# Optimization experiments

Hardware: AMD Instinct MI355X
Metric: run time of the kernel (lower is better)

The kernel has to match this reference:

```python
import jax, jax.numpy as jnp
import numpy as np

B, N, D = 4, 1024, 1024
H, KV, HD = 16, 4, 64
S, CTX = 128, 2048
MLPD = 4096
NITER, DT = 2, 0.1


def _rms(x, w, eps=1e-6):
    return x * jax.lax.rsqrt(jnp.mean(x * x, axis=-1, keepdims=True) + eps) * w


def _gelu(x):
    return jax.nn.gelu(x, approximate=False)  # torch nn.GELU() is exact erf


def _rope(q, k, cos, sin):
    # q: [B,H,N,HD], cos/sin: [N, HD//2]; interleaved-half RoPE as in source
    q1, q2 = q[..., ::2], q[..., 1::2]
    k1, k2 = k[..., ::2], k[..., 1::2]
    c = cos[None, None]
    s = sin[None, None]
    q_rot = jnp.concatenate([q1 * c - q2 * s, q1 * s + q2 * c], axis=-1)
    k_rot = jnp.concatenate([k1 * c - k2 * s, k1 * s + k2 * c], axis=-1)
    return q_rot, k_rot


def setup_inputs():
    key = jax.random.key(0)
    ks = jax.random.split(key, 24)
    rn = lambda k, shp, s=0.02: jax.random.normal(k, shp, jnp.float32) * s
    inv = 1.0 / (10000.0 ** (jnp.arange(0, HD, 2, dtype=jnp.float32) / HD))  # [HD//2]
    ang = jnp.arange(N, dtype=jnp.float32)[:, None] * inv[None, :]
    return {
        'x': jax.random.normal(ks[0], (B, N, D), jnp.float32),
        'c': jax.random.normal(ks[1], (B, D), jnp.float32),
        'context': jax.random.normal(ks[2], (B, S, CTX), jnp.float32),
        'cos': jnp.cos(ang), 'sin': jnp.sin(ang),
        'wq': rn(ks[3], (D, D)), 'wk': rn(ks[4], (D, KV * HD)),
        'wv': rn(ks[5], (D, KV * HD)), 'wo': rn(ks[6], (D, D)),
        'cwq': rn(ks[7], (D, D)), 'cwk': rn(ks[8], (CTX, D)),
        'cwv': rn(ks[9], (CTX, D)), 'cwo': rn(ks[10], (D, D)),
        'fc1_w': rn(ks[11], (D, MLPD)), 'fc1_b': jnp.zeros((MLPD,), jnp.float32),
        'fc2_w': rn(ks[12], (MLPD, D)), 'fc2_b': jnp.zeros((D,), jnp.float32),
        'ada_w': rn(ks[13], (D, 6 * D)), 'ada_b': jnp.zeros((6 * D,), jnp.float32),
        'n1': jnp.ones((D,), jnp.float32), 'n2': jnp.ones((D,), jnp.float32), 'n3': jnp.ones((D,), jnp.float32),
        'int_w': jnp.full((D,), 0.5, jnp.float32), 'mu': jnp.zeros((D,), jnp.float32),
        'hg1_w': rn(ks[14], (D, D // 4)), 'hg1_b': jnp.zeros((D // 4,), jnp.float32),
        'hg2_w': rn(ks[15], (D // 4, 1)), 'hg2_b': jnp.zeros((1,), jnp.float32),
        'ct1_w': rn(ks[16], (2 * D, D // 2)), 'ct1_b': jnp.zeros((D // 2,), jnp.float32),
        'ct2_w': rn(ks[17], (D // 2, 3 * D)), 'ct2_b': jnp.zeros((3 * D,), jnp.float32),
        'rf1_w': rn(ks[18], (D, 2 * D)), 'rf1_b': jnp.zeros((2 * D,), jnp.float32),
        'rf2_w': rn(ks[19], (2 * D, D)), 'rf2_b': jnp.zeros((D,), jnp.float32),
    }


def _forward(x, c, context, cos, sin, wq, wk, wv, wo, cwq, cwk, cwv, cwo,
             fc1_w, fc1_b, fc2_w, fc2_b, ada_w, ada_b, n1, n2, n3, int_w, mu,
             hg1_w, hg1_b, hg2_w, hg2_b, ct1_w, ct1_b, ct2_w, ct2_b,
             rf1_w, rf1_b, rf2_w, rf2_b):
    scale = HD ** -0.5
    # AdaLN-Zero modulation from timestep conditioning c: [B, 6D]
    mod = jax.nn.silu(c) @ ada_w + ada_b
    sh_msa, sc_msa, g_msa, sh_mlp, sc_mlp, g_mlp = jnp.split(mod, 6, axis=-1)
    # --- GQA self-attention with RoPE ---
    h = _rms(x, n1) * (1.0 + sc_msa[:, None, :]) + sh_msa[:, None, :]
    q = (h @ wq).reshape(B, N, H, HD).transpose(0, 2, 1, 3)
    k = (h @ wk).reshape(B, N, KV, HD).transpose(0, 2, 1, 3)
    v = (h @ wv).reshape(B, N, KV, HD).transpose(0, 2, 1, 3)
    q, k = _rope(q, k, cos, sin)
    k = jnp.repeat(k, H // KV, axis=1)  # repeat_interleave over head dim
    v = jnp.repeat(v, H // KV, axis=1)
    attn = jax.nn.softmax(jnp.einsum('bhnd,bhmd->bhnm', q, k) * scale, axis=-1)
    sa = jnp.einsum('bhnm,bhmd->bhnd', attn, v).transpose(0, 2, 1, 3).reshape(B, N, D) @ wo
    x = x + g_msa[:, None, :] * sa
    # --- cross-attention (text conditioning) ---
    h2 = _rms(x, n2)
    qc = (h2 @ cwq).reshape(B, N, H, HD).transpose(0, 2, 1, 3)
    kc = (context @ cwk).reshape(B, S, H, HD).transpose(0, 2, 1, 3)
    vc = (context @ cwv).reshape(B, S, H, HD).transpose(0, 2, 1, 3)
    ca = jax.nn.softmax(jnp.einsum('bhnd,bhsd->bhns', qc, kc) * scale, axis=-1)
    xa = jnp.einsum('bhns,bhsd->bhnd', ca, vc).transpose(0, 2, 1, 3).reshape(B, N, D) @ cwo
    x = x + xa
    # --- AdaLN-modulated MLP ---
    h3 = _rms(x, n3) * (1.0 + sc_mlp[:, None, :]) + sh_mlp[:, None, :]
    m = _gelu(h3 @ fc1_w + fc1_b) @ fc2_w + fc2_b
    x = x + g_mlp[:, None, :] * m
    # --- IntegratorNeuron: damped-oscillator halting dynamics ---
    vst = jnp.zeros_like(x)
    integ = x
    halt_probs = []
    for _ in range(NITER):
        ctrl = _gelu(jnp.concatenate([integ, vst], axis=-1) @ ct1_w + ct1_b) @ ct2_w + ct2_b
        a_raw, b_raw, g_raw = jnp.split(ctrl, 3, axis=-1)
        alpha = jax.nn.sigmoid(a_raw)
        beta = jax.nn.softplus(b_raw)
        gate = jax.nn.sigmoid(g_raw)
        v_next = alpha * vst - beta * (integ - mu)
        x_next = integ + DT * gate * v_next
        hp = jax.nn.sigmoid(_gelu(x_next @ hg1_w + hg1_b) @ hg2_w + hg2_b)  # [B,N,1]
        refined = _gelu(x_next @ rf1_w + rf1_b) @ rf2_w + rf2_b
        integ = integ + hp * refined * int_w
        vst = v_next
        halt_probs.append(hp)
    return integ, jnp.stack(halt_probs, axis=1)


def reference(x, c, context, cos, sin, wq, wk, wv, wo, cwq, cwk, cwv, cwo,
              fc1_w, fc1_b, fc2_w, fc2_b, ada_w, ada_b, n1, n2, n3, int_w, mu,
              hg1_w, hg1_b, hg2_w, hg2_b, ct1_w, ct1_b, ct2_w, ct2_b,
              rf1_w, rf1_b, rf2_w, rf2_b):
    return _forward(x, c, context, cos, sin, wq, wk, wv, wo, cwq, cwk, cwv, cwo,
                    fc1_w, fc1_b, fc2_w, fc2_b, ada_w, ada_b, n1, n2, n3, int_w, mu,
                    hg1_w, hg1_b, hg2_w, hg2_b, ct1_w, ct1_b, ct2_w, ct2_b,
                    rf1_w, rf1_b, rf2_w, rf2_b)
```

## Files before the change

### kernel.cpp

```cpp
#include <hip/hip_runtime.h>
#include <hip/hip_bf16.h>
#include <math.h>

typedef __hip_bfloat16 bf16;
typedef unsigned short ushort;
typedef __bf16 bf16x8 __attribute__((ext_vector_type(8)));
typedef unsigned short u16x8 __attribute__((ext_vector_type(8)));
typedef float f32x4 __attribute__((ext_vector_type(4)));

#define BB 4
#define NN 1024
#define DD 1024
#define HH 16
#define KVH 4
#define HDIM 64
#define SS 128
#define CTXD 2048
#define MLPDIM 4096

__device__ __forceinline__ float bf2f(bf16 v){ return __bfloat162float(v); }
__device__ __forceinline__ bf16 f2bf(float v){ return __float2bfloat16(v); }
__device__ __forceinline__ ushort fbits(float v){ bf16 h = __float2bfloat16(v); return *(ushort*)&h; }
__device__ __forceinline__ float ubf(ushort u){ unsigned int x = ((unsigned int)u) << 16; float f; *(unsigned int*)&f = x; return f; }
__device__ __forceinline__ float sigmf_(float x){ return 1.f/(1.f+expf(-x)); }
__device__ __forceinline__ float geluf_(float x){ return 0.5f*x*(1.f+erff(x*0.70710678118f)); }

typedef const __attribute__((address_space(1))) void* gas_t;
typedef __attribute__((address_space(3))) void* las_t;
__device__ __forceinline__ void gl2lds16(const void* g, void* l){
  __builtin_amdgcn_global_load_lds((gas_t)g, (las_t)l, 16, 0, 0);
}

__global__ void k_copy4(const float4* __restrict__ in, float4* __restrict__ out, int n4){
  int i = blockIdx.x*256 + threadIdx.x;
  if (i < n4) out[i] = in[i];
}
__global__ void k_f2bfv(const float* __restrict__ in, bf16* __restrict__ out, int n){
  int i = blockIdx.x*256 + threadIdx.x;
  if (i < n) out[i] = f2bf(in[i]);
}
__global__ void k_silu(const float* __restrict__ c, float* __restrict__ out, int n){
  int i = blockIdx.x*256 + threadIdx.x;
  if (i < n){ float v = c[i]; out[i] = v*sigmf_(v); }
}
__global__ void k_zero16(unsigned short* __restrict__ p, int n){
  int i = blockIdx.x*256 + threadIdx.x;
  if (i < n) p[i] = 0;
}

__global__ __launch_bounds__(256) void k_wt(const float* __restrict__ in, bf16* __restrict__ out, int K, int N){
  __shared__ float t[64][65];
  int bn = blockIdx.x*64, bk = blockIdx.y*64;
  int tid = threadIdx.x;
  int c4 = (tid & 15)*4, r = tid >> 4;
  #pragma unroll
  for (int i = 0; i < 4; ++i){
    float4 v = *(const float4*)(in + (size_t)(bk + r + i*16)*N + bn + c4);
    t[c4+0][r+i*16] = v.x; t[c4+1][r+i*16] = v.y; t[c4+2][r+i*16] = v.z; t[c4+3][r+i*16] = v.w;
  }
  __syncthreads();
  int n = tid >> 2, k16 = (tid & 3)*16;
  bf16* orow = out + (size_t)(bn + n)*K + bk + k16;
  #pragma unroll
  for (int j = 0; j < 16; ++j) orow[j] = f2bf(t[n][k16 + j]);
}

__global__ void k_adab(const float* __restrict__ b, float* __restrict__ mod, int n){
  int idx = blockIdx.x*256 + threadIdx.x;
  if (idx < n) mod[idx] = b[idx % 6144];
}
__global__ __launch_bounds__(256) void k_ada2(const float* __restrict__ sc, const float* __restrict__ w,
                       float* __restrict__ mod){
  __shared__ float sl[4][32];
  int tid = threadIdx.x;
  int col4 = blockIdx.x*1024 + tid*4;
  int k0 = blockIdx.y*32;
  if (tid < 128) sl[tid >> 5][tid & 31] = sc[(tid >> 5)*DD + k0 + (tid & 31)];
  __syncthreads();
  f32x4 acc[4] = {};
  for (int kk = 0; kk < 32; ++kk){
    const float4 wv4 = *(const float4*)(w + (size_t)(k0 + kk)*6144 + col4);
    #pragma unroll
    for (int b = 0; b < 4; ++b){
      float s = sl[b][kk];
      acc[b][0] += s*wv4.x; acc[b][1] += s*wv4.y; acc[b][2] += s*wv4.z; acc[b][3] += s*wv4.w;
    }
  }
  #pragma unroll
  for (int b = 0; b < 4; ++b)
    #pragma unroll
    for (int j = 0; j < 4; ++j)
      atomicAdd(&mod[(size_t)b*6144 + col4 + j], acc[b][j]);
}

__global__ __launch_bounds__(256) void k_rms(const float* __restrict__ X, const float* __restrict__ w,
                      const float* __restrict__ mod, int sc_off, int sh_off,
                      bf16* __restrict__ out, int use_mod){
  __shared__ float red[256];
  int row = blockIdx.x;
  int b = row >> 10;
  int tid = threadIdx.x;
  const float* xr = X + (size_t)row*DD;
  float s = 0.f;
  #pragma unroll
  for (int i = 0; i < 4; ++i){ float v = xr[tid + i*256]; s += v*v; }
  red[tid] = s; __syncthreads();
  for (int st = 128; st > 0; st >>= 1){ if (tid < st) red[tid] += red[tid+st]; __syncthreads(); }
  float rstd = rsqrtf(red[0]*(1.f/DD) + 1e-6f);
  bf16* orow = out + (size_t)row*DD;
  const float* mrow = use_mod ? (mod + (size_t)b*6*DD) : nullptr;
  #pragma unroll
  for (int i = 0; i < 4; ++i){
    int d = tid + i*256;
    float v = xr[d]*rstd*w[d];
    if (use_mod) v = v*(1.f + mrow[sc_off + d]) + mrow[sh_off + d];
    orow[d] = f2bf(v);
  }
}

__global__ __launch_bounds__(256,2) void k_mm2(const ushort* __restrict__ A, const ushort* __restrict__ BT,
                      const float* __restrict__ bias, ushort* __restrict__ C,
                      int M, int N, int K, int act){
  __shared__ ushort As[128*64];
  __shared__ ushort Bs[128*64];
  int tid = threadIdx.x, lane = tid & 63, wv = tid >> 6;
  int l15 = lane & 15, quad = lane >> 4;
  int bm = blockIdx.y*128, bn = blockIdx.x*128;
  int wm = (wv & 1)*64, wn = (wv >> 1)*64;
  int lr = lane >> 3, lc = lane & 7;
  int ksw = (lc ^ lr) << 3;
  f32x4 acc[4][4] = {};
  const ushort* Abase = A  + (size_t)(bm + wv*32 + lr)*K + ksw;
  const ushort* Bbase = BT + (size_t)(bn + wv*32 + lr)*K + ksw;
  ushort* AsW = As + wv*2048;
  ushort* BsW = Bs + wv*2048;
  int swr = (l15 & 7) << 3;
  for (int k0 = 0; k0 < K; k0 += 64){
    #pragma unroll
    for (int i = 0; i < 4; ++i){
      gl2lds16(Abase + k0 + (size_t)(i*8)*K, AsW + i*512);
      gl2lds16(Bbase + k0 + (size_t)(i*8)*K, BsW + i*512);
    }
    __syncthreads();
    #pragma unroll
    for (int ks = 0; ks < 2; ++ks){
      bf16x8 af[4], bfr[4];
      #pragma unroll
      for (int mi = 0; mi < 4; ++mi){
        int r = wm + mi*16 + l15;
        af[mi] = __builtin_bit_cast(bf16x8, *(const uint4*)(As + r*64 + ((ks*32 + quad*8) ^ swr)));
      }
      #pragma unroll
      for (int nj = 0; nj < 4; ++nj){
        int r = wn + nj*16 + l15;
        bfr[nj] = __builtin_bit_cast(bf16x8, *(const uint4*)(Bs + r*64 + ((ks*32 + quad*8) ^ swr)));
      }
      #pragma unroll
      for (int mi = 0; mi < 4; ++mi)
        #pragma unroll
        for (int nj = 0; nj < 4; ++nj)
          acc[mi][nj] = __builtin_amdgcn_mfma_f32_16x16x32_bf16(af[mi], bfr[nj], acc[mi][nj], 0, 0, 0);
    }
    __syncthreads();
  }
  #pragma unroll
  for (int nj = 0; nj < 4; ++nj){
    int col = bn + wn + nj*16 + l15;
    float bv = bias ? bias[col] : 0.f;
    #pragma unroll
    for (int mi = 0; mi < 4; ++mi){
      #pragma unroll
      for (int r = 0; r < 4; ++r){
        int row = bm + wm + mi*16 + quad*4 + r;
        float v = acc[mi][nj][r] + bv;
        if (act) v = geluf_(v);
        C[(size_t)row*N + col] = fbits(v);
      }
    }
  }
}

__global__ void k_rope(const bf16* __restrict__ in, const float* __restrict__ cw,
                       const float* __restrict__ sw, bf16* __restrict__ out, int NHp, int n){
  int idx = blockIdx.x*256 + threadIdx.x;
  if (idx >= n) return;
  int d2 = idx & 31; int t = idx >> 5;
  int nn = t % NN; t /= NN; int h = t % NHp; int b = t / NHp;
  const bf16* base = in + ((size_t)((b*NN+nn)*NHp + h))*HDIM;
  float e = bf2f(base[2*d2]), o = bf2f(base[2*d2+1]);
  float c = cw[nn*32 + d2], s = sw[nn*32 + d2];
  bf16* ob = out + ((size_t)((b*NHp+h)*NN + nn))*HDIM;
  ob[d2]      = f2bf(e*c - o*s);
  ob[32 + d2] = f2bf(e*s + o*c);
}

__global__ void k_tr(const bf16* __restrict__ in, bf16* __restrict__ out, int T, int NHp, int n){
  int idx = blockIdx.x*256 + threadIdx.x;
  if (idx >= n) return;
  int d = idx & 63; int t = idx >> 6;
  int h = t % NHp; t /= NHp; int tok = t % T; int b = t / T;
  out[((size_t)((b*NHp+h)*T + tok))*64 + d] = in[idx];
}

__global__ void k_trv(const bf16* __restrict__ in, bf16* __restrict__ out, int T, int NHp, int n){
  int idx = blockIdx.x*256 + threadIdx.x;
  if (idx >= n) return;
  int d = idx & 63; int t = idx >> 6;
  int h = t % NHp; t /= NHp; int tok = t % T; int b = t / T;
  out[((size_t)(b*NHp+h)*64 + d)*T + tok] = in[idx];
}

__global__ __launch_bounds__(256) void k_fattn(const ushort* __restrict__ Q, const ushort* __restrict__ K,
                      const ushort* __restrict__ V, ushort* __restrict__ O,
                      int NH, int NKV, int Nq, int Nk, float scale){
  __shared__ ushort Kt[64*72];
  __shared__ ushort Vt[64*72];
  __shared__ ushort Ps[4][16*72];
  int tid = threadIdx.x, lane = tid & 63, wv = tid >> 6;
  int l15 = lane & 15, quad = lane >> 4;
  int nqt = Nq >> 6;
  int qt = blockIdx.x % nqt; int t = blockIdx.x / nqt; int h = t % NH; int b = t / NH;
  int kvh = h / (NH / NKV);
  const ushort* Kb = K + (size_t)(b*NKV+kvh)*Nk*64;
  const ushort* Vb = V + (size_t)(b*NKV+kvh)*64*Nk;
  const ushort* Qp = Q + ((size_t)((b*NH+h)*Nq + qt*64 + wv*16 + l15))*64;
  bf16x8 qf0 = __builtin_bit_cast(bf16x8, *(const uint4*)(Qp + quad*8));
  bf16x8 qf1 = __builtin_bit_cast(bf16x8, *(const uint4*)(Qp + 32 + quad*8));
  f32x4 acc[4] = {};
  float m_run[4] = {-1e30f,-1e30f,-1e30f,-1e30f};
  float l_run[4] = {0.f,0.f,0.f,0.f};
  ushort* Pw = Ps[wv];
  for (int t0 = 0; t0 < Nk; t0 += 64){
    #pragma unroll
    for (int i = 0; i < 2; ++i){
      int c = tid + i*256; int row = c >> 3; int k8 = (c & 7) << 3;
      *(uint4*)(Kt + row*72 + k8) = *(const uint4*)(Kb + (size_t)(t0+row)*64 + k8);
      *(uint4*)(Vt + row*72 + k8) = *(const uint4*)(Vb + (size_t)row*Nk + t0 + k8);
    }
    __syncthreads();
    f32x4 s[4] = {};
    #pragma unroll
    for (int nj = 0; nj < 4; ++nj){
      bf16x8 kf0 = __builtin_bit_cast(bf16x8, *(const uint4*)(Kt + (nj*16+l15)*72 + quad*8));
      s[nj] = __builtin_amdgcn_mfma_f32_16x16x32_bf16(qf0, kf0, s[nj], 0, 0, 0);
      bf16x8 kf1 = __builtin_bit_cast(bf16x8, *(const uint4*)(Kt + (nj*16+l15)*72 + 32 + quad*8));
      s[nj] = __builtin_amdgcn_mfma_f32_16x16x32_bf16(qf1, kf1, s[nj], 0, 0, 0);
    }
    #pragma unroll
    for (int nj = 0; nj < 4; ++nj)
      #pragma unroll
      for (int r = 0; r < 4; ++r) s[nj][r] *= scale;
    float al[4];
    #pragma unroll
    for (int r = 0; r < 4; ++r){
      float tm = fmaxf(fmaxf(s[0][r], s[1][r]), fmaxf(s[2][r], s[3][r]));
      #pragma unroll
      for (int off = 8; off; off >>= 1) tm = fmaxf(tm, __shfl_xor(tm, off, 64));
      float mn = fmaxf(m_run[r], tm);
      al[r] = expf(m_run[r] - mn);
      m_run[r] = mn;
      float ts = 0.f;
      #pragma unroll
      for (int nj = 0; nj < 4; ++nj){ float p = expf(s[nj][r] - mn); s[nj][r] = p; ts += p; }
      #pragma unroll
      for (int off = 8; off; off >>= 1) ts += __shfl_xor(ts, off, 64);
      l_run[r] = l_run[r]*al[r] + ts;
    }
    #pragma unroll
    for (int nj = 0; nj < 4; ++nj){
      #pragma unroll
      for (int r = 0; r < 4; ++r){
        acc[nj][r] *= al[r];
        Pw[(quad*4+r)*72 + nj*16 + l15] = fbits(s[nj][r]);
      }
    }
    bf16x8 pf0 = __builtin_bit_cast(bf16x8, *(const uint4*)(Pw + l15*72 + quad*8));
    bf16x8 pf1 = __builtin_bit_cast(bf16x8, *(const uint4*)(Pw + l15*72 + 32 + quad*8));
    #pragma unroll
    for (int nj = 0; nj < 4; ++nj){
      bf16x8 vf0 = __builtin_bit_cast(bf16x8, *(const uint4*)(Vt + (nj*16+l15)*72 + quad*8));
      acc[nj] = __builtin_amdgcn_mfma_f32_16x16x32_bf16(pf0, vf0, acc[nj], 0, 0, 0);
      bf16x8 vf1 = __builtin_bit_cast(bf16x8, *(const uint4*)(Vt + (nj*16+l15)*72 + 32 + quad*8));
      acc[nj] = __builtin_amdgcn_mfma_f32_16x16x32_bf16(pf1, vf1, acc[nj], 0, 0, 0);
    }
    __syncthreads();
  }
  float inv[4];
  #pragma unroll
  for (int r = 0; r < 4; ++r) inv[r] = 1.f / l_run[r];
  int nbase = qt*64 + wv*16 + quad*4;
  #pragma unroll
  for (int r = 0; r < 4; ++r){
    size_t ob = ((size_t)((b*Nq + nbase + r)*NH + h))*64;
    #pragma unroll
    for (int nj = 0; nj < 4; ++nj)
      O[ob + nj*16 + l15] = fbits(acc[nj][r]*inv[r]);
  }
}

__global__ void k_resid(float* __restrict__ X, const bf16* __restrict__ val,
                        const float* __restrict__ mod, int goff, int n){
  int i = blockIdx.x*256 + threadIdx.x;
  if (i >= n) return;
  float g = 1.f;
  if (mod){ int b = i >> 20; int d = i & 1023; g = mod[b*6144 + goff + d]; }
  X[i] += g*bf2f(val[i]);
}

__global__ void k_concat(const float* __restrict__ X, const bf16* __restrict__ V,
                         bf16* __restrict__ C, int n){
  int i = blockIdx.x*256 + threadIdx.x;
  if (i >= n) return;
  int row = i >> 11, col = i & 2047;
  C[i] = (col < 1024) ? f2bf(X[(size_t)row*1024 + col]) : V[(size_t)row*1024 + col - 1024];
}

__global__ void k_ctrl(const bf16* __restrict__ ctrl, const float* __restrict__ X,
                       bf16* __restrict__ VST, bf16* __restrict__ XN,
                       const float* __restrict__ mu, int n){
  int i = blockIdx.x*256 + threadIdx.x;
  if (i >= n) return;
  int row = i >> 10, d = i & 1023;
  const bf16* cr = ctrl + (size_t)row*3072;
  float alpha = sigmf_(bf2f(cr[d]));
  float braw  = bf2f(cr[1024 + d]);
  float beta  = fmaxf(braw, 0.f) + log1pf(expf(-fabsf(braw)));
  float gate  = sigmf_(bf2f(cr[2048 + d]));
  float vn = alpha*bf2f(VST[i]) - beta*(X[i] - mu[d]);
  VST[i] = f2bf(vn);
  XN[i]  = f2bf(X[i] + 0.1f*gate*vn);
}

__global__ __launch_bounds__(64) void k_hg2(const bf16* __restrict__ hin, const float* __restrict__ w,
                     const float* __restrict__ bb, float* __restrict__ hp,
                     float* __restrict__ oout, int it){
  int r = blockIdx.x; int lane = threadIdx.x;
  const bf16* hr = hin + (size_t)r*256;
  float s = 0.f;
  #pragma unroll
  for (int i = 0; i < 4; ++i) s += bf2f(hr[lane + i*64])*w[lane + i*64];
  for (int off = 32; off; off >>= 1) s += __shfl_xor(s, off, 64);
  if (lane == 0){
    float v = sigmf_(s + bb[0]);
    hp[r] = v;
    int b = r >> 10, nn = r & 1023;
    oout[((size_t)(b*2 + it) << 10) + nn] = v;
  }
}

__global__ void k_integ(float* __restrict__ X, const float* __restrict__ hp,
                        const bf16* __restrict__ rf, const float* __restrict__ iw, int n){
  int i = blockIdx.x*256 + threadIdx.x;
  if (i >= n) return;
  int row = i >> 10, d = i & 1023;
  X[i] += hp[row]*bf2f(rf[i])*iw[d];
}

extern "C" void kernel_launch(void* const* d_in, const int* in_sizes, int n_in,
                              void* d_out, int out_size, void* d_ws, size_t ws_size,
                              hipStream_t stream) {
  const float* x_in  = (const float*)d_in[0];
  const float* c_in  = (const float*)d_in[1];
  const float* ctx_in= (const float*)d_in[2];
  const float* cosw  = (const float*)d_in[3];
  const float* sinw  = (const float*)d_in[4];
  const float* wq    = (const float*)d_in[5];
  const float* wk    = (const float*)d_in[6];
  const float* wv    = (const float*)d_in[7];
  const float* wo    = (const float*)d_in[8];
  const float* cwq   = (const float*)d_in[9];
  const float* cwk   = (const float*)d_in[10];
  const float* cwv   = (const float*)d_in[11];
  const float* cwo   = (const float*)d_in[12];
  const float* fc1_w = (const float*)d_in[13];
  const float* fc1_b = (const float*)d_in[14];
  const float* fc2_w = (const float*)d_in[15];
  const float* fc2_b = (const float*)d_in[16];
  const float* ada_w = (const float*)d_in[17];
  const float* ada_b = (const float*)d_in[18];
  const float* n1    = (const float*)d_in[19];
  const float* n2    = (const float*)d_in[20];
  const float* n3    = (const float*)d_in[21];
  const float* int_w = (const float*)d_in[22];
  const float* mu    = (const float*)d_in[23];
  const float* hg1_w = (const float*)d_in[24];
  const float* hg1_b = (const float*)d_in[25];
  const float* hg2_w = (const float*)d_in[26];
  const float* hg2_b = (const float*)d_in[27];
  const float* ct1_w = (const float*)d_in[28];
  const float* ct1_b = (const float*)d_in[29];
  const float* ct2_w = (const float*)d_in[30];
  const float* ct2_b = (const float*)d_in[31];
  const float* rf1_w = (const float*)d_in[32];
  const float* rf1_b = (const float*)d_in[33];
  const float* rf2_w = (const float*)d_in[34];
  const float* rf2_b = (const float*)d_in[35];

  float* out_f  = (float*)d_out;
  float* out_hp = out_f + (size_t)BB*NN*DD;

  char* wsb = (char*)d_ws;
  const size_t Mi = 1u << 20;
  float* X  = (float*)wsb;
  bf16*  Hh = (bf16*)(wsb + 16*Mi);
  bf16*  Qb = (bf16*)(wsb + 24*Mi);
  bf16*  R  = (bf16*)(wsb + 32*Mi);
  bf16*  QR  = R;
  bf16*  SAb = R + 4*Mi;
  bf16*  KP  = R + 8*Mi;
  bf16*  VP  = R + 9*Mi;
  bf16*  KR  = R + 10*Mi;
  bf16*  VR  = R + 11*Mi;
  bf16*  CTXB= R + 12*Mi;
  bf16*  BIG = R;
  bf16*  CT1 = R + 12*Mi;
  bf16*  HG1 = R + 12*Mi;
  bf16*  RFO = R + 8*Mi;
  float* SIL = (float*)(wsb + 64*Mi);
  float* MOD = SIL + 4096;
  float* HP  = MOD + 24576;
  bf16*  VST = Qb;
  bf16*  XN  = Hh;
  bf16* WT   = (bf16*)(wsb + 65*Mi);
  bf16* wqT  = WT;
  bf16* wkT  = wqT  + 1048576;
  bf16* wvT  = wkT  + 262144;
  bf16* woT  = wvT  + 262144;
  bf16* cwqT = woT  + 1048576;
  bf16* cwkT = cwqT + 1048576;
  bf16* cwvT = cwkT + 2097152;
  bf16* cwoT = cwvT + 2097152;
  bf16* fc1T = cwoT + 1048576;
  bf16* fc2T = fc1T + 4194304;
  bf16* ct1T = fc2T + 4194304;
  bf16* ct2T = ct1T + 1048576;
  bf16* rf1T = ct2T + 1572864;
  bf16* rf2T = rf1T + 2097152;
  bf16* hg1T = rf2T + 2097152;

  const int NT = BB*NN*DD;
  const float scale = 0.125f;
  #define G1(n) dim3(((n)+255)/256), dim3(256)
  #define WTR(src,dst,K,N) k_wt<<<dim3((N)/64,(K)/64), dim3(256), 0, stream>>>((src),(dst),(K),(N))
  #define MM(Aptr,BTptr,biasptr,Cptr,M,N,K,act) \
    k_mm2<<<dim3((N)/128,(M)/128), dim3(256), 0, stream>>>((const ushort*)(Aptr),(const ushort*)(BTptr),(biasptr),(ushort*)(Cptr),(M),(N),(K),(act))

  WTR(wq,   wqT, 1024, 1024);
  WTR(wk,   wkT, 1024, 256);
  WTR(wv,   wvT, 1024, 256);
  WTR(wo,   woT, 1024, 1024);
  WTR(cwq,  cwqT,1024, 1024);
  WTR(cwk,  cwkT,2048, 1024);
  WTR(cwv,  cwvT,2048, 1024);
  WTR(cwo,  cwoT,1024, 1024);
  WTR(fc1_w,fc1T,1024, 4096);
  WTR(fc2_w,fc2T,4096, 1024);
  WTR(ct1_w,ct1T,2048, 512);
  WTR(ct2_w,ct2T,512,  3072);
  WTR(rf1_w,rf1T,1024, 2048);
  WTR(rf2_w,rf2T,2048, 1024);
  WTR(hg1_w,hg1T,1024, 256);

  k_copy4<<<G1(NT/4), 0, stream>>>((const float4*)x_in, (float4*)X, NT/4);
  k_silu<<<G1(BB*DD), 0, stream>>>(c_in, SIL, BB*DD);
  k_adab<<<G1(BB*6144), 0, stream>>>(ada_b, MOD, BB*6144);
  k_ada2<<<dim3(6,32), dim3(256), 0, stream>>>(SIL, ada_w, MOD);

  k_rms<<<dim3(4096), dim3(256), 0, stream>>>(X, n1, MOD, DD, 0, Hh, 1);
  MM(Hh, wqT, nullptr, Qb, 4096, 1024, 1024, 0);
  MM(Hh, wkT, nullptr, KP, 4096, 256, 1024, 0);
  MM(Hh, wvT, nullptr, VP, 4096, 256, 1024, 0);
  k_rope<<<G1(BB*HH*NN*32), 0, stream>>>(Qb, cosw, sinw, QR, HH, BB*HH*NN*32);
  k_rope<<<G1(BB*KVH*NN*32), 0, stream>>>(KP, cosw, sinw, KR, KVH, BB*KVH*NN*32);
  k_trv<<<G1(BB*NN*KVH*64), 0, stream>>>(VP, VR, NN, KVH, BB*NN*KVH*64);
  k_fattn<<<dim3(BB*HH*(NN/64)), dim3(256), 0, stream>>>((const ushort*)QR, (const ushort*)KR,
      (const ushort*)VR, (ushort*)SAb, HH, KVH, NN, NN, scale);
  MM(SAb, woT, nullptr, Hh, 4096, 1024, 1024, 0);
  k_resid<<<G1(NT), 0, stream>>>(X, Hh, MOD, 2*DD, NT);

  k_rms<<<dim3(4096), dim3(256), 0, stream>>>(X, n2, nullptr, 0, 0, Hh, 0);
  MM(Hh, cwqT, nullptr, Qb, 4096, 1024, 1024, 0);
  k_tr<<<G1(NT), 0, stream>>>(Qb, QR, NN, HH, NT);
  k_f2bfv<<<G1(BB*SS*CTXD), 0, stream>>>(ctx_in, CTXB, BB*SS*CTXD);
  MM(CTXB, cwkT, nullptr, KP, 512, 1024, 2048, 0);
  MM(CTXB, cwvT, nullptr, VP, 512, 1024, 2048, 0);
  k_tr<<<G1(BB*SS*HH*64), 0, stream>>>(KP, KR, SS, HH, BB*SS*HH*64);
  k_trv<<<G1(BB*SS*HH*64), 0, stream>>>(VP, VR, SS, HH, BB*SS*HH*64);
  k_fattn<<<dim3(BB*HH*(NN/64)), dim3(256), 0, stream>>>((const ushort*)QR, (const ushort*)KR,
      (const ushort*)VR, (ushort*)SAb, HH, HH, NN, SS, scale);
  MM(SAb, cwoT, nullptr, Hh, 4096, 1024, 1024, 0);
  k_resid<<<G1(NT), 0, stream>>>(X, Hh, nullptr, 0, NT);

  k_rms<<<dim3(4096), dim3(256), 0, stream>>>(X, n3, MOD, 4*DD, 3*DD, Hh, 1);
  MM(Hh, fc1T, fc1_b, BIG, 4096, 4096, 1024, 1);
  MM(BIG, fc2T, fc2_b, Qb, 4096, 1024, 4096, 0);
  k_resid<<<G1(NT), 0, stream>>>(X, Qb, MOD, 5*DD, NT);

  k_zero16<<<G1(NT), 0, stream>>>((unsigned short*)VST, NT);
  for (int it = 0; it < 2; ++it){
    k_concat<<<G1(2*NT), 0, stream>>>(X, VST, BIG, 2*NT);
    MM(BIG, ct1T, ct1_b, CT1, 4096, 512, 2048, 1);
    MM(CT1, ct2T, ct2_b, BIG, 4096, 3072, 512, 0);
    k_ctrl<<<G1(NT), 0, stream>>>(BIG, X, VST, XN, mu, NT);
    MM(XN, hg1T, hg1_b, HG1, 4096, 256, 1024, 1);
    k_hg2<<<dim3(4096), dim3(64), 0, stream>>>(HG1, hg2_w, hg2_b, HP, out_hp, it);
    MM(XN, rf1T, rf1_b, BIG, 4096, 2048, 1024, 1);
    MM(BIG, rf2T, rf2_b, RFO, 4096, 1024, 2048, 0);
    k_integ<<<G1(NT), 0, stream>>>(X, HP, RFO, int_w, NT);
  }
  k_copy4<<<G1(NT/4), 0, stream>>>((const float4*)X, (float4*)out_f, NT/4);
  #undef G1
  #undef WTR
  #undef MM
}
```

Before: 1.172 ms.

## Add half-width GEMM tile for narrow outputs and swizzle flash-attention LDS loads

Adds a 128x64-tile GEMM variant with launch bounds for two blocks per CU, and uses it for the narrow-N projections (K/V, context K/V, ct1, hg1). This raises the block count on small grids that previously underfilled the GPU. Flash attention now stages K/V into LDS with direct global-to-LDS copies and an XOR swizzle instead of padding. It also folds the softmax scale into Q once, which rounds Q to bf16 after scaling, and raises wave priority around the MFMA sections. The risks are lower per-block reuse in the smaller GEMM tiles and a slight numerical change from pre-scaling Q in bf16.

```diff
diff --git a/kernel.cpp b/kernel.cpp
--- a/kernel.cpp
+++ b/kernel.cpp
@@ -180,6 +180,69 @@
   }
 }
 
+__global__ __launch_bounds__(256,2) void k_mm2h(const ushort* __restrict__ A, const ushort* __restrict__ BT,
+                      const float* __restrict__ bias, ushort* __restrict__ C,
+                      int M, int N, int K, int act){
+  __shared__ ushort As[128*64];
+  __shared__ ushort Bs[64*64];
+  int tid = threadIdx.x, lane = tid & 63, wv = tid >> 6;
+  int l15 = lane & 15, quad = lane >> 4;
+  int bm = blockIdx.y*128, bn = blockIdx.x*64;
+  int wm = wv*32;
+  int lr = lane >> 3, lc = lane & 7;
+  int ksw = (lc ^ lr) << 3;
+  f32x4 acc[2][4] = {};
+  const ushort* Abase = A  + (size_t)(bm + wv*32 + lr)*K + ksw;
+  const ushort* Bbase = BT + (size_t)(bn + wv*16 + lr)*K + ksw;
+  ushort* AsW = As + wv*2048;
+  ushort* BsW = Bs + wv*1024;
+  int swr = (l15 & 7) << 3;
+  for (int k0 = 0; k0 < K; k0 += 64){
+    #pragma unroll
+    for (int i = 0; i < 4; ++i)
+      gl2lds16(Abase + k0 + (size_t)(i*8)*K, AsW + i*512);
+    #pragma unroll
+    for (int i = 0; i < 2; ++i)
+      gl2lds16(Bbase + k0 + (size_t)(i*8)*K, BsW + i*512);
+    __syncthreads();
+    #pragma unroll
+    for (int ks = 0; ks < 2; ++ks){
+      bf16x8 af[2], bfr[4];
+      #pragma unroll
+      for (int mi = 0; mi < 2; ++mi){
+        int r = wm + mi*16 + l15;
+        af[mi] = __builtin_bit_cast(bf16x8, *(const uint4*)(As + r*64 + ((ks*32 + quad*8) ^ swr)));
+      }
+      #pragma unroll
+      for (int nj = 0; nj < 4; ++nj){
+        int r = nj*16 + l15;
+        bfr[nj] = __builtin_bit_cast(bf16x8, *(const uint4*)(Bs + r*64 + ((ks*32 + quad*8) ^ swr)));
+      }
+      #pragma unroll
+      for (int mi = 0; mi < 2; ++mi)
+        #pragma unroll
+        for (int nj = 0; nj < 4; ++nj)
+          acc[mi][nj] = __builtin_amdgcn_mfma_f32_16x16x32_bf16(af[mi], bfr[nj], acc[mi][nj], 0, 0, 0);
+    }
+    __syncthreads();
+  }
+  #pragma unroll
+  for (int nj = 0; nj < 4; ++nj){
+    int col = bn + nj*16 + l15;
+    float bv = bias ? bias[col] : 0.f;
+    #pragma unroll
+    for (int mi = 0; mi < 2; ++mi){
+      #pragma unroll
+      for (int r = 0; r < 4; ++r){
+        int row = bm + wm + mi*16 + quad*4 + r;
+        float v = acc[mi][nj][r] + bv;
+        if (act) v = geluf_(v);
+        C[(size_t)row*N + col] = fbits(v);
+      }
+    }
+  }
+}
+
 __global__ void k_rope(const bf16* __restrict__ in, const float* __restrict__ cw,
                        const float* __restrict__ sw, bf16* __restrict__ out, int NHp, int n){
   int idx = blockIdx.x*256 + threadIdx.x;
@@ -213,43 +276,51 @@
 __global__ __launch_bounds__(256) void k_fattn(const ushort* __restrict__ Q, const ushort* __restrict__ K,
                       const ushort* __restrict__ V, ushort* __restrict__ O,
                       int NH, int NKV, int Nq, int Nk, float scale){
-  __shared__ ushort Kt[64*72];
-  __shared__ ushort Vt[64*72];
+  __shared__ ushort Kt[64*64];
+  __shared__ ushort Vt[64*64];
   __shared__ ushort Ps[4][16*72];
   int tid = threadIdx.x, lane = tid & 63, wv = tid >> 6;
   int l15 = lane & 15, quad = lane >> 4;
+  int lr = lane >> 3, lc = lane & 7;
+  int ksw = (lc ^ lr) << 3;
+  int swr = (l15 & 7) << 3;
   int nqt = Nq >> 6;
   int qt = blockIdx.x % nqt; int t = blockIdx.x / nqt; int h = t % NH; int b = t / NH;
   int kvh = h / (NH / NKV);
-  const ushort* Kb = K + (size_t)(b*NKV+kvh)*Nk*64;
-  const ushort* Vb = V + (size_t)(b*NKV+kvh)*64*Nk;
+  const ushort* Kb = K + (size_t)(b*NKV+kvh)*Nk*64 + ksw;
+  const ushort* Vb = V + (size_t)(b*NKV+kvh)*64*Nk + ksw;
   const ushort* Qp = Q + ((size_t)((b*NH+h)*Nq + qt*64 + wv*16 + l15))*64;
-  bf16x8 qf0 = __builtin_bit_cast(bf16x8, *(const uint4*)(Qp + quad*8));
-  bf16x8 qf1 = __builtin_bit_cast(bf16x8, *(const uint4*)(Qp + 32 + quad*8));
+  uint4 qraw0 = *(const uint4*)(Qp + quad*8);
+  uint4 qraw1 = *(const uint4*)(Qp + 32 + quad*8);
+  u16x8 q0 = __builtin_bit_cast(u16x8, qraw0), q1 = __builtin_bit_cast(u16x8, qraw1);
+  #pragma unroll
+  for (int j = 0; j < 8; ++j){ q0[j] = fbits(ubf(q0[j])*scale); q1[j] = fbits(ubf(q1[j])*scale); }
+  bf16x8 qf0 = __builtin_bit_cast(bf16x8, q0);
+  bf16x8 qf1 = __builtin_bit_cast(bf16x8, q1);
   f32x4 acc[4] = {};
   float m_run[4] = {-1e30f,-1e30f,-1e30f,-1e30f};
   float l_run[4] = {0.f,0.f,0.f,0.f};
   ushort* Pw = Ps[wv];
+  int wrow = wv*16;
   for (int t0 = 0; t0 < Nk; t0 += 64){
     #pragma unroll
     for (int i = 0; i < 2; ++i){
-      int c = tid + i*256; int row = c >> 3; int k8 = (c & 7) << 3;
-      *(uint4*)(Kt + row*72 + k8) = *(const uint4*)(Kb + (size_t)(t0+row)*64 + k8);
-      *(uint4*)(Vt + row*72 + k8) = *(const uint4*)(Vb + (size_t)row*Nk + t0 + k8);
+      int row = wrow + i*8 + lr;
+      gl2lds16(Kb + (size_t)(t0+row)*64, Kt + (wrow + i*8)*64);
+      gl2lds16(Vb + (size_t)row*Nk + t0, Vt + (wrow + i*8)*64);
     }
     __syncthreads();
     f32x4 s[4] = {};
+    __builtin_amdgcn_s_setprio(1);
     #pragma unroll
     for (int nj = 0; nj < 4; ++nj){
-      bf16x8 kf0 = __builtin_bit_cast(bf16x8, *(const uint4*)(Kt + (nj*16+l15)*72 + quad*8));
+      const ushort* kr = Kt + (nj*16+l15)*64;
+      bf16x8 kf0 = __builtin_bit_cast(bf16x8, *(const uint4*)(kr + ((quad*8) ^ swr)));
       s[nj] = __builtin_amdgcn_mfma_f32_16x16x32_bf16(qf0, kf0, s[nj], 0, 0, 0);
-      bf16x8 kf1 = __builtin_bit_cast(bf16x8, *(const uint4*)(Kt + (nj*16+l15)*72 + 32 + quad*8));
+      bf16x8 kf1 = __builtin_bit_cast(bf16x8, *(const uint4*)(kr + ((32 + quad*8) ^ swr)));
       s[nj] = __builtin_amdgcn_mfma_f32_16x16x32_bf16(qf1, kf1, s[nj], 0, 0, 0);
     }
-    #pragma unroll
-    for (int nj = 0; nj < 4; ++nj)
-      #pragma unroll
-      for (int r = 0; r < 4; ++r) s[nj][r] *= scale;
+    __builtin_amdgcn_s_setprio(0);
     float al[4];
     #pragma unroll
     for (int r = 0; r < 4; ++r){
@@ -276,13 +347,16 @@
     }
     bf16x8 pf0 = __builtin_bit_cast(bf16x8, *(const uint4*)(Pw + l15*72 + quad*8));
     bf16x8 pf1 = __builtin_bit_cast(bf16x8, *(const uint4*)(Pw + l15*72 + 32 + quad*8));
+    __builtin_amdgcn_s_setprio(1);
     #pragma unroll
     for (int nj = 0; nj < 4; ++nj){
-      bf16x8 vf0 = __builtin_bit_cast(bf16x8, *(const uint4*)(Vt + (nj*16+l15)*72 + quad*8));
+      const ushort* vr = Vt + (nj*16+l15)*64;
+      bf16x8 vf0 = __builtin_bit_cast(bf16x8, *(const uint4*)(vr + ((quad*8) ^ swr)));
       acc[nj] = __builtin_amdgcn_mfma_f32_16x16x32_bf16(pf0, vf0, acc[nj], 0, 0, 0);
-      bf16x8 vf1 = __builtin_bit_cast(bf16x8, *(const uint4*)(Vt + (nj*16+l15)*72 + 32 + quad*8));
+      bf16x8 vf1 = __builtin_bit_cast(bf16x8, *(const uint4*)(vr + ((32 + quad*8) ^ swr)));
       acc[nj] = __builtin_amdgcn_mfma_f32_16x16x32_bf16(pf1, vf1, acc[nj], 0, 0, 0);
     }
+    __builtin_amdgcn_s_setprio(0);
     __syncthreads();
   }
   float inv[4];
@@ -444,6 +518,8 @@
   #define WTR(src,dst,K,N) k_wt<<<dim3((N)/64,(K)/64), dim3(256), 0, stream>>>((src),(dst),(K),(N))
   #define MM(Aptr,BTptr,biasptr,Cptr,M,N,K,act) \
     k_mm2<<<dim3((N)/128,(M)/128), dim3(256), 0, stream>>>((const ushort*)(Aptr),(const ushort*)(BTptr),(biasptr),(ushort*)(Cptr),(M),(N),(K),(act))
+  #define MMH(Aptr,BTptr,biasptr,Cptr,M,N,K,act) \
+    k_mm2h<<<dim3((N)/64,(M)/128), dim3(256), 0, stream>>>((const ushort*)(Aptr),(const ushort*)(BTptr),(biasptr),(ushort*)(Cptr),(M),(N),(K),(act))
 
   WTR(wq,   wqT, 1024, 1024);
   WTR(wk,   wkT, 1024, 256);
@@ -468,8 +544,8 @@
 
   k_rms<<<dim3(4096), dim3(256), 0, stream>>>(X, n1, MOD, DD, 0, Hh, 1);
   MM(Hh, wqT, nullptr, Qb, 4096, 1024, 1024, 0);
-  MM(Hh, wkT, nullptr, KP, 4096, 256, 1024, 0);
-  MM(Hh, wvT, nullptr, VP, 4096, 256, 1024, 0);
+  MMH(Hh, wkT, nullptr, KP, 4096, 256, 1024, 0);
+  MMH(Hh, wvT, nullptr, VP, 4096, 256, 1024, 0);
   k_rope<<<G1(BB*HH*NN*32), 0, stream>>>(Qb, cosw, sinw, QR, HH, BB*HH*NN*32);
   k_rope<<<G1(BB*KVH*NN*32), 0, stream>>>(KP, cosw, sinw, KR, KVH, BB*KVH*NN*32);
   k_trv<<<G1(BB*NN*KVH*64), 0, stream>>>(VP, VR, NN, KVH, BB*NN*KVH*64);
@@ -482,8 +558,8 @@
   MM(Hh, cwqT, nullptr, Qb, 4096, 1024, 1024, 0);
   k_tr<<<G1(NT), 0, stream>>>(Qb, QR, NN, HH, NT);
   k_f2bfv<<<G1(BB*SS*CTXD), 0, stream>>>(ctx_in, CTXB, BB*SS*CTXD);
-  MM(CTXB, cwkT, nullptr, KP, 512, 1024, 2048, 0);
-  MM(CTXB, cwvT, nullptr, VP, 512, 1024, 2048, 0);
+  MMH(CTXB, cwkT, nullptr, KP, 512, 1024, 2048, 0);
+  MMH(CTXB, cwvT, nullptr, VP, 512, 1024, 2048, 0);
   k_tr<<<G1(BB*SS*HH*64), 0, stream>>>(KP, KR, SS, HH, BB*SS*HH*64);
   k_trv<<<G1(BB*SS*HH*64), 0, stream>>>(VP, VR, SS, HH, BB*SS*HH*64);
   k_fattn<<<dim3(BB*HH*(NN/64)), dim3(256), 0, stream>>>((const ushort*)QR, (const ushort*)KR,
@@ -499,10 +575,10 @@
   k_zero16<<<G1(NT), 0, stream>>>((unsigned short*)VST, NT);
   for (int it = 0; it < 2; ++it){
     k_concat<<<G1(2*NT), 0, stream>>>(X, VST, BIG, 2*NT);
-    MM(BIG, ct1T, ct1_b, CT1, 4096, 512, 2048, 1);
+    MMH(BIG, ct1T, ct1_b, CT1, 4096, 512, 2048, 1);
     MM(CT1, ct2T, ct2_b, BIG, 4096, 3072, 512, 0);
     k_ctrl<<<G1(NT), 0, stream>>>(BIG, X, VST, XN, mu, NT);
-    MM(XN, hg1T, hg1_b, HG1, 4096, 256, 1024, 1);
+    MMH(XN, hg1T, hg1_b, HG1, 4096, 256, 1024, 1);
     k_hg2<<<dim3(4096), dim3(64), 0, stream>>>(HG1, hg2_w, hg2_b, HP, out_hp, it);
     MM(XN, rf1T, rf1_b, BIG, 4096, 2048, 1024, 1);
     MM(BIG, rf2T, rf2_b, RFO, 4096, 1024, 2048, 0);
@@ -512,4 +588,5 @@
   #undef G1
   #undef WTR
   #undef MM
-}
+  #undef MMH
+}
```

Measured after the change: 1.125 ms. 1.04x faster.
